# Performance work log

Measured on AMD Instinct MI355X. Metric: run time of the kernel, lower is better.

The kernel has to match this reference:

```python
import jax, jax.numpy as jnp
import numpy as np

K_PRE_NMS = 2000      # number of top-scoring candidates fed to NMS
IOU_THRESHOLD = 0.5
IMAGE_SIZE = 800.0


def decode_boxes(deltas, locations, stride):
    """Faithful fcos_apply_deltas_to_locations (incl. the all(-1) special case
    and the swapped-y-coordinate convention of the source)."""
    d = deltas * stride
    x, y = locations[:, 0], locations[:, 1]
    boxes = jnp.stack([x - d[:, 0], y - d[:, 1], x + d[:, 2], y + d[:, 3]], axis=1)
    all_bg = jnp.all(deltas == -1)
    degen = jnp.stack([x, y, x, y], axis=1)
    return jnp.where(all_bg, degen, boxes)


def nms_keep_mask(boxes_sorted, iou_threshold):
    """Sequential NMS on score-descending-sorted boxes. Reproduces the source's
    exact (quirky) IoU math: y1=boxes[:,3], y2=boxes[:,1], w/h via abs().
    Returns bool keep mask aligned with the sorted order."""
    K = boxes_sorted.shape[0]
    x1, y1 = boxes_sorted[:, 0], boxes_sorted[:, 3]
    x2, y2 = boxes_sorted[:, 2], boxes_sorted[:, 1]
    area = (x2 - x1) * (y2 - y1)
    idx = jnp.arange(K)

    def body(i, state):
        active, keep = state
        is_kept = active[i]
        keep = keep.at[i].set(is_kept)
        xx1 = jnp.maximum(x1[i], x1)
        yy1 = jnp.minimum(y1[i], y1)
        xx2 = jnp.minimum(x2[i], x2)
        yy2 = jnp.maximum(y2[i], y2)
        inter = jnp.abs(xx2 - xx1) * jnp.abs(yy2 - yy1)
        iou = inter / (area[i] + area - inter)
        suppress = is_kept & (iou > iou_threshold) & (idx > i)
        return active & ~suppress, keep

    active0 = jnp.ones((K,), dtype=bool)
    keep0 = jnp.zeros((K,), dtype=bool)
    _, keep = jax.lax.fori_loop(0, K, body, (active0, keep0))
    return keep


def setup_inputs() -> dict:
    key = jax.random.key(0)
    k1, k2, k3 = jax.random.split(key, 3)
    N, C = 1048576, 20
    deltas = jax.random.normal(k1, (N, 4), dtype=jnp.float32) * 4.0 + 8.0
    locations = jax.random.uniform(k2, (N, 2), dtype=jnp.float32) * IMAGE_SIZE
    logits = jax.random.normal(k3, (N, C), dtype=jnp.float32)
    return {"deltas": deltas, "locations": locations, "logits": logits, "stride": 8}


def reference(deltas, locations, logits, stride):
    # 1) box delta decode (all N locations)
    boxes = decode_boxes(deltas, locations, stride)
    # 2) per-location best class score / class id
    probs = jax.nn.sigmoid(logits)              # [N, C]
    cls_scores = jnp.max(probs, axis=1)         # [N]
    class_ids = jnp.argmax(probs, axis=1)       # [N]
    # 3) pre-NMS top-k
    top_scores, top_idx = jax.lax.top_k(cls_scores, K_PRE_NMS)
    cand_boxes = boxes[top_idx]                 # [K, 4]
    cand_cls = class_ids[top_idx]               # [K]
    # 4) class-offset trick (class_spec_nms)
    max_coord = jnp.max(cand_boxes)
    offsets = cand_cls.astype(cand_boxes.dtype) * (max_coord + 1.0)
    boxes_for_nms = cand_boxes + offsets[:, None]
    # 5) sort by score descending (top_k already sorted; argsort is faithful to nms())
    order = jnp.argsort(-top_scores)
    keep = nms_keep_mask(boxes_for_nms[order], IOU_THRESHOLD)
    return cand_boxes[order], top_scores[order], cand_cls[order], keep
```

## Files before the change

### kernel.cpp

```cpp
#include <hip/hip_runtime.h>
#include <stdint.h>
#include <math.h>

#pragma clang fp contract(off)

#define N_ROWS 1048576
#define N_CLS  20
#define K_TOP  2000
#define CAND_MAX 8192
#define NBINS  4096
#define H_COPIES 4
#define DELTA_ULP 4096u

#define SC_CNT   0
#define SC_MAXK  1
#define SC_DONE  2
#define SC_BAR   3
#define SC_FLAG  4

static constexpr size_t OFF_MKEY = 0;
static constexpr size_t OFF_CLS  = OFF_MKEY + 4ull * N_ROWS;
static constexpr size_t OFF_HIST = OFF_CLS + (size_t)N_ROWS;
static constexpr size_t OFF_SCAL = OFF_HIST + 4ull * H_COPIES * NBINS;
static constexpr size_t OFF_GRP  = OFF_SCAL + 64;
static constexpr size_t OFF_CAND = OFF_GRP + 256;
static constexpr size_t OFF_MASK = OFF_CAND + 8ull * CAND_MAX;

__device__ __forceinline__ uint32_t mono_key(float f) {
    uint32_t u = __float_as_uint(f);
    return u ^ ((u & 0x80000000u) ? 0xFFFFFFFFu : 0x80000000u);
}
__device__ __forceinline__ float mono_inv(uint32_t k) {
    uint32_t u = (k & 0x80000000u) ? (k ^ 0x80000000u) : ~k;
    return __uint_as_float(u);
}

__global__ __launch_bounds__(256) void k_scoremax(const float* __restrict__ logits,
                                                  uint32_t* __restrict__ mkey,
                                                  uint8_t* __restrict__ cls,
                                                  uint32_t* __restrict__ zreg) {
    int t = threadIdx.x, b = blockIdx.x;
    if (b < 8) {
#pragma unroll
        for (int k = 0; k < 8; ++k) zreg[b * 256 + t + k * 2048] = 0;
        if (b == 7 && t < 80) zreg[16384 + t] = 0;
    }
    size_t r0 = (size_t)b * 1024 + t;
    const float4* p0 = (const float4*)(logits + r0 * N_CLS);
    const float4* p1 = (const float4*)(logits + (r0 + 256) * N_CLS);
    const float4* p2 = (const float4*)(logits + (r0 + 512) * N_CLS);
    const float4* p3 = (const float4*)(logits + (r0 + 768) * N_CLS);
    float4 a0 = p0[0], a1 = p0[1], a2 = p0[2], a3 = p0[3], a4 = p0[4];
    float4 b0 = p1[0], b1 = p1[1], b2 = p1[2], b3 = p1[3], b4 = p1[4];
    float4 c0 = p2[0], c1 = p2[1], c2 = p2[2], c3 = p2[3], c4 = p2[4];
    float4 d0 = p3[0], d1 = p3[1], d2 = p3[2], d3 = p3[3], d4 = p3[4];
    __builtin_amdgcn_sched_barrier(0);

#define CK(mm, cc, val, idx) if ((val) > mm) { mm = (val); cc = (idx); }
    float mA = a0.x; int cA = 0;
    CK(mA, cA, a0.y, 1)  CK(mA, cA, a0.z, 2)  CK(mA, cA, a0.w, 3)
    CK(mA, cA, a1.x, 4)  CK(mA, cA, a1.y, 5)  CK(mA, cA, a1.z, 6)  CK(mA, cA, a1.w, 7)
    CK(mA, cA, a2.x, 8)  CK(mA, cA, a2.y, 9)  CK(mA, cA, a2.z, 10) CK(mA, cA, a2.w, 11)
    CK(mA, cA, a3.x, 12) CK(mA, cA, a3.y, 13) CK(mA, cA, a3.z, 14) CK(mA, cA, a3.w, 15)
    CK(mA, cA, a4.x, 16) CK(mA, cA, a4.y, 17) CK(mA, cA, a4.z, 18) CK(mA, cA, a4.w, 19)
    float mB = b0.x; int cB = 0;
    CK(mB, cB, b0.y, 1)  CK(mB, cB, b0.z, 2)  CK(mB, cB, b0.w, 3)
    CK(mB, cB, b1.x, 4)  CK(mB, cB, b1.y, 5)  CK(mB, cB, b1.z, 6)  CK(mB, cB, b1.w, 7)
    CK(mB, cB, b2.x, 8)  CK(mB, cB, b2.y, 9)  CK(mB, cB, b2.z, 10) CK(mB, cB, b2.w, 11)
    CK(mB, cB, b3.x, 12) CK(mB, cB, b3.y, 13) CK(mB, cB, b3.z, 14) CK(mB, cB, b3.w, 15)
    CK(mB, cB, b4.x, 16) CK(mB, cB, b4.y, 17) CK(mB, cB, b4.z, 18) CK(mB, cB, b4.w, 19)
    float mC = c0.x; int cC = 0;
    CK(mC, cC, c0.y, 1)  CK(mC, cC, c0.z, 2)  CK(mC, cC, c0.w, 3)
    CK(mC, cC, c1.x, 4)  CK(mC, cC, c1.y, 5)  CK(mC, cC, c1.z, 6)  CK(mC, cC, c1.w, 7)
    CK(mC, cC, c2.x, 8)  CK(mC, cC, c2.y, 9)  CK(mC, cC, c2.z, 10) CK(mC, cC, c2.w, 11)
    CK(mC, cC, c3.x, 12) CK(mC, cC, c3.y, 13) CK(mC, cC, c3.z, 14) CK(mC, cC, c3.w, 15)
    CK(mC, cC, c4.x, 16) CK(mC, cC, c4.y, 17) CK(mC, cC, c4.z, 18) CK(mC, cC, c4.w, 19)
    float mD = d0.x; int cD = 0;
    CK(mD, cD, d0.y, 1)  CK(mD, cD, d0.z, 2)  CK(mD, cD, d0.w, 3)
    CK(mD, cD, d1.x, 4)  CK(mD, cD, d1.y, 5)  CK(mD, cD, d1.z, 6)  CK(mD, cD, d1.w, 7)
    CK(mD, cD, d2.x, 8)  CK(mD, cD, d2.y, 9)  CK(mD, cD, d2.z, 10) CK(mD, cD, d2.w, 11)
    CK(mD, cD, d3.x, 12) CK(mD, cD, d3.y, 13) CK(mD, cD, d3.z, 14) CK(mD, cD, d3.w, 15)
    CK(mD, cD, d4.x, 16) CK(mD, cD, d4.y, 17) CK(mD, cD, d4.z, 18) CK(mD, cD, d4.w, 19)
#undef CK

    mkey[r0]       = mono_key(mA);  cls[r0]       = (uint8_t)cA;
    mkey[r0 + 256] = mono_key(mB);  cls[r0 + 256] = (uint8_t)cB;
    mkey[r0 + 512] = mono_key(mC);  cls[r0 + 512] = (uint8_t)cC;
    mkey[r0 + 768] = mono_key(mD);  cls[r0 + 768] = (uint8_t)cD;
}

__global__ __launch_bounds__(256) void k_histcompact(const uint32_t* __restrict__ mkey,
                                                     uint32_t* __restrict__ hist,
                                                     uint32_t* __restrict__ scal,
                                                     unsigned long long* __restrict__ cand) {
    __shared__ uint32_t hh[NBINS];
    __shared__ uint64_t stg[1024];
    __shared__ uint32_t bc;
    __shared__ uint32_t cnt, gbase;
    __shared__ int islast;
    int t = threadIdx.x, b = blockIdx.x;
    int lane = t & 63;
    if (t == 0) cnt = 0;
    for (int i = t; i < NBINS; i += 256) hh[i] = 0;
    __syncthreads();

    const uint4* m4 = (const uint4*)mkey;
    size_t base = (size_t)b * 1024;
    uint4 v0 = m4[base + t], v1 = m4[base + 256 + t];
    uint4 v2 = m4[base + 512 + t], v3 = m4[base + 768 + t];
    atomicAdd(&hh[v0.x >> 20], 1u); atomicAdd(&hh[v0.y >> 20], 1u);
    atomicAdd(&hh[v0.z >> 20], 1u); atomicAdd(&hh[v0.w >> 20], 1u);
    atomicAdd(&hh[v1.x >> 20], 1u); atomicAdd(&hh[v1.y >> 20], 1u);
    atomicAdd(&hh[v1.z >> 20], 1u); atomicAdd(&hh[v1.w >> 20], 1u);
    atomicAdd(&hh[v2.x >> 20], 1u); atomicAdd(&hh[v2.y >> 20], 1u);
    atomicAdd(&hh[v2.z >> 20], 1u); atomicAdd(&hh[v2.w >> 20], 1u);
    atomicAdd(&hh[v3.x >> 20], 1u); atomicAdd(&hh[v3.y >> 20], 1u);
    atomicAdd(&hh[v3.z >> 20], 1u); atomicAdd(&hh[v3.w >> 20], 1u);
    __syncthreads();

    uint32_t cp = (uint32_t)((b & (H_COPIES - 1)) << 12);
    unsigned long long dummy = 0;
    for (int i = 0; i < 16; ++i) {
        uint32_t h = hh[t * 16 + i];
        if (h) dummy += atomicAdd(&hist[cp + t * 16 + i], h);
    }
    asm volatile("" :: "v"(dummy));
    asm volatile("s_waitcnt vmcnt(0) lgkmcnt(0)" ::: "memory");
    __syncthreads();
    if (t == 0) {
        uint32_t old = atomicAdd(&scal[SC_BAR], 1u);
        islast = (old == 255u) ? 1 : 0;
    }
    __syncthreads();

    if (islast) {
        uint32_t bv[16]; uint32_t ct = 0;
#pragma unroll
        for (int i = 0; i < 16; ++i) {
            uint32_t s = 0;
#pragma unroll
            for (int k = 0; k < H_COPIES; ++k) s += atomicAdd(&hist[(k << 12) + t * 16 + i], 0u);
            bv[i] = s; ct += s;
        }
        hh[t] = ct;
        __syncthreads();
        for (int off = 1; off < 256; off <<= 1) {
            uint32_t v = (t + off < 256) ? hh[t + off] : 0;
            __syncthreads();
            hh[t] += v;
            __syncthreads();
        }
        if (hh[t] >= (uint32_t)K_TOP && (t == 255 || hh[t + 1] < (uint32_t)K_TOP)) {
            uint32_t cum = (t == 255) ? 0u : hh[t + 1];
            int i = 15;
            for (; i >= 0; --i) { cum += bv[i]; if (cum >= (uint32_t)K_TOP) break; }
            if (i < 0) i = 0;
            uint32_t tk = ((uint32_t)(t * 16 + i)) << 20;
            uint32_t Tk = (tk > DELTA_ULP) ? (tk - DELTA_ULP) : 0u;
            atomicExch(&scal[SC_FLAG], Tk + 1u);
        }
    }
    for (;;) {
        if (t == 0) bc = atomicAdd(&scal[SC_FLAG], 0u);
        __syncthreads();
        if (bc != 0u) break;
        __builtin_amdgcn_s_sleep(32);
    }
    uint32_t T = bc - 1u;

#define CSLOT(u, roff) {                                                         \
        uint32_t uu = (u);                                                       \
        bool pass = uu >= T;                                                     \
        unsigned long long bal = __ballot(pass);                                 \
        if (bal) {                                                               \
            uint32_t wbase = 0;                                                  \
            if (lane == 0) wbase = atomicAdd(&cnt, (uint32_t)__popcll(bal));     \
            wbase = __shfl(wbase, 0);                                            \
            if (pass) {                                                          \
                uint32_t pos = wbase + (uint32_t)__popcll(bal & ((1ull << lane) - 1ull)); \
                if (pos < 1024) {                                                \
                    float m = mono_inv(uu);                                      \
                    float ef = (float)exp(-(double)m);                           \
                    float s = 1.0f / (1.0f + ef);                                \
                    stg[pos] = ((uint64_t)(~__float_as_uint(s)) << 32) | (roff); \
                }                                                                \
            }                                                                    \
        }                                                                        \
    }
    uint32_t rb = (uint32_t)((base + t) * 4);
    CSLOT(v0.x, rb + 0) CSLOT(v0.y, rb + 1) CSLOT(v0.z, rb + 2) CSLOT(v0.w, rb + 3)
    rb = (uint32_t)((base + 256 + t) * 4);
    CSLOT(v1.x, rb + 0) CSLOT(v1.y, rb + 1) CSLOT(v1.z, rb + 2) CSLOT(v1.w, rb + 3)
    rb = (uint32_t)((base + 512 + t) * 4);
    CSLOT(v2.x, rb + 0) CSLOT(v2.y, rb + 1) CSLOT(v2.z, rb + 2) CSLOT(v2.w, rb + 3)
    rb = (uint32_t)((base + 768 + t) * 4);
    CSLOT(v3.x, rb + 0) CSLOT(v3.y, rb + 1) CSLOT(v3.z, rb + 2) CSLOT(v3.w, rb + 3)
#undef CSLOT
    __syncthreads();
    uint32_t n = cnt; if (n > 1024) n = 1024;
    if (t == 0 && n) gbase = atomicAdd(&scal[SC_CNT], n);
    __syncthreads();
    if (n) {
        uint32_t gb = gbase;
        for (uint32_t i = t; i < n; i += 256) {
            uint32_t pos = gb + i;
            if (pos < (uint32_t)CAND_MAX) cand[pos] = stg[i];
        }
    }
}

__global__ __launch_bounds__(256) void k_rank(const unsigned long long* __restrict__ cand,
                                              uint32_t* __restrict__ scal,
                                              const float* __restrict__ deltas,
                                              const float* __restrict__ locs,
                                              const int* __restrict__ stridep,
                                              const uint8_t* __restrict__ cls,
                                              float* __restrict__ out) {
    __shared__ uint64_t keys[CAND_MAX];
    int t = threadIdx.x;
    uint32_t M = scal[SC_CNT];
    if (M > (uint32_t)CAND_MAX) M = CAND_MAX;
    for (uint32_t i = t; i < M; i += 256) keys[i] = cand[i];
    __syncthreads();
    int wid = t >> 6, lane = t & 63;
    float stridef = (float)(*stridep);
    float wmx = -3.4e38f;
    for (uint32_t c = (uint32_t)blockIdx.x * 4 + wid; c < M; c += 1024) {
        uint64_t myk = keys[c];
        uint32_t r = 0;
        uint32_t j = lane;
        for (; j + 192 < M; j += 256) {
            uint64_t k0 = keys[j], k1 = keys[j + 64], k2 = keys[j + 128], k3 = keys[j + 192];
            r += (uint32_t)(k0 < myk) + (uint32_t)(k1 < myk)
               + (uint32_t)(k2 < myk) + (uint32_t)(k3 < myk);
        }
        for (; j < M; j += 64) r += (keys[j] < myk) ? 1u : 0u;
#pragma unroll
        for (int o = 32; o > 0; o >>= 1) r += __shfl_down(r, o);
        if (lane == 0 && r < (uint32_t)K_TOP) {
            uint32_t row = (uint32_t)myk & (N_ROWS - 1);
            float s = __uint_as_float(~(uint32_t)(myk >> 32));
            float4 dl = ((const float4*)deltas)[row];
            float2 lc = ((const float2*)locs)[row];
            float d0 = dl.x * stridef, d1 = dl.y * stridef, d2 = dl.z * stridef, d3 = dl.w * stridef;
            float b0f = lc.x - d0, b1f = lc.y - d1, b2f = lc.x + d2, b3f = lc.y + d3;
            float4 bx = { b0f, b1f, b2f, b3f };
            *(float4*)&out[4 * r] = bx;
            out[8000 + r] = s;
            out[10000 + r] = (float)cls[row];
            wmx = fmaxf(wmx, fmaxf(fmaxf(b0f, b1f), fmaxf(b2f, b3f)));
        }
    }
    if (lane == 0) atomicMax(&scal[SC_MAXK], mono_key(wmx));
}

__global__ __launch_bounds__(256) void k_maskscan(const float* __restrict__ out_ro,
                                                  uint32_t* __restrict__ scal,
                                                  uint64_t* __restrict__ mask,
                                                  unsigned long long* __restrict__ grp,
                                                  float* __restrict__ out) {
    __shared__ uint64_t wb[4][32];
    __shared__ int lastdone;
    int t = threadIdx.x;
    int lane = t & 63;
    int wid = t >> 6;
    int i = blockIdx.x * 4 + wid;
    float off1 = mono_inv(scal[SC_MAXK]) + 1.0f;
    float4 boxi = *(const float4*)&out_ro[4 * i];
    float oi = out_ro[10000 + i] * off1;
    float x1i = boxi.x + oi, y2i = boxi.y + oi, x2i = boxi.z + oi, y1i = boxi.w + oi;
    float ai = (x2i - x1i) * (y2i - y1i);
    uint64_t any = 0;
    for (int jb = 0; jb < 32; ++jb) {
        int j = jb * 64 + lane;
        bool sup = false;
        if (j < K_TOP && j > i) {
            float4 boxj = *(const float4*)&out_ro[4 * j];
            float oj = out_ro[10000 + j] * off1;
            float x1j = boxj.x + oj, y2j = boxj.y + oj, x2j = boxj.z + oj, y1j = boxj.w + oj;
            float aj = (x2j - x1j) * (y2j - y1j);
            float xx1 = fmaxf(x1i, x1j);
            float yy1 = fminf(y1i, y1j);
            float xx2 = fminf(x2i, x2j);
            float yy2 = fmaxf(y2i, y2j);
            float inter = fabsf(xx2 - xx1) * fabsf(yy2 - yy1);
            float iou = inter / ((ai + aj) - inter);
            sup = iou > 0.5f;
        }
        unsigned long long bits = __ballot(sup);
        if (lane == 0) wb[wid][jb] = bits;
        any |= bits;
    }
    unsigned long long dummy = 0;
    if (lane == 0 && any) {
        for (int jb = 0; jb < 32; ++jb)
            dummy += atomicExch(&mask[(size_t)i * 32 + jb], wb[wid][jb]);
        dummy += atomicOr(&grp[i >> 6], 1ull << (i & 63));
    }
    asm volatile("" :: "v"(dummy));
    asm volatile("s_waitcnt vmcnt(0) lgkmcnt(0)" ::: "memory");
    __syncthreads();
    if (t == 0) {
        unsigned old = atomicAdd(&scal[SC_DONE], 1u);
        lastdone = (old == (unsigned)(gridDim.x - 1)) ? 1 : 0;
    }
    __syncthreads();
    if (!lastdone) return;

    if (t < 64) {
        int l = t;
        uint64_t g = (l < 32) ? atomicOr(&grp[l], 0ull) : 0ull;
        uint64_t active = ~0ull;
        if (__ballot(g != 0ull)) {
            for (int gg = 0; gg < 32; ++gg) {
                uint64_t nz = __shfl(g, gg);
                while (nz) {
                    int b = __ffsll((long long)nz) - 1;
                    nz &= nz - 1;
                    int ii = gg * 64 + b;
                    uint64_t aw = __shfl(active, gg);
                    bool kept = (aw >> b) & 1ull;
                    uint64_t m = (l < 32) ? atomicOr(&mask[(size_t)ii * 32 + l], 0ull) : 0ull;
                    if (kept) active &= ~m;
                }
            }
        }
        if (l < 32) {
            int limit = K_TOP - l * 64;
            int nvec = limit < 64 ? limit / 4 : 16;
            for (int v = 0; v < nvec; ++v) {
                float4 f;
                f.x = ((active >> (4 * v + 0)) & 1ull) ? 1.0f : 0.0f;
                f.y = ((active >> (4 * v + 1)) & 1ull) ? 1.0f : 0.0f;
                f.z = ((active >> (4 * v + 2)) & 1ull) ? 1.0f : 0.0f;
                f.w = ((active >> (4 * v + 3)) & 1ull) ? 1.0f : 0.0f;
                *(float4*)&out[12000 + l * 64 + 4 * v] = f;
            }
        }
    }
}

extern "C" void kernel_launch(void* const* d_in, const int* in_sizes, int n_in,
                              void* d_out, int out_size, void* d_ws, size_t ws_size,
                              hipStream_t stream) {
    const float* deltas = (const float*)d_in[0];
    const float* locs   = (const float*)d_in[1];
    const float* logits = (const float*)d_in[2];
    const int*   stridep = (const int*)d_in[3];
    float* out = (float*)d_out;
    char* ws = (char*)d_ws;

    uint32_t* mkey = (uint32_t*)(ws + OFF_MKEY);
    uint8_t*  cls  = (uint8_t*)(ws + OFF_CLS);
    uint32_t* hist = (uint32_t*)(ws + OFF_HIST);
    uint32_t* scal = (uint32_t*)(ws + OFF_SCAL);
    unsigned long long* grp = (unsigned long long*)(ws + OFF_GRP);
    unsigned long long* cand = (unsigned long long*)(ws + OFF_CAND);
    uint64_t* mask = (uint64_t*)(ws + OFF_MASK);

    k_scoremax<<<dim3(1024), dim3(256), 0, stream>>>(logits, mkey, cls, hist);
    k_histcompact<<<dim3(256), dim3(256), 0, stream>>>(mkey, hist, scal, cand);
    k_rank<<<dim3(256), dim3(256), 0, stream>>>(cand, scal, deltas, locs, stridep, cls, out);
    k_maskscan<<<dim3(500), dim3(256), 0, stream>>>(out, scal, mask, grp, out);
}
```

Baseline: 90.07 us.

## Fuse histogram-compact and rank kernels via a second grid-wide spin barrier

Merges k_histcompact and k_rank into one persistent kernel, k_select. A second atomic counter barrier (SC_BAR2/SC_FLAG2) publishes the final candidate count, and all blocks then reload candidates from global memory with atomic reads into a reused 64KB shared buffer. This removes one kernel launch and the gap between the two kernels. In exchange it depends on all 256 blocks being co-resident, adds atomic writes and reads on the candidate array, and caps the key count slightly below CAND_MAX to make room for scalars in shared memory.

```diff
diff --git a/kernel.cpp b/kernel.cpp
--- a/kernel.cpp
+++ b/kernel.cpp
@@ -8,6 +8,7 @@
 #define N_CLS  20
 #define K_TOP  2000
 #define CAND_MAX 8192
+#define KEYS_MAX 8184
 #define NBINS  4096
 #define H_COPIES 4
 #define DELTA_ULP 4096u
@@ -17,6 +18,8 @@
 #define SC_DONE  2
 #define SC_BAR   3
 #define SC_FLAG  4
+#define SC_BAR2  5
+#define SC_FLAG2 6
 
 static constexpr size_t OFF_MKEY = 0;
 static constexpr size_t OFF_CLS  = OFF_MKEY + 4ull * N_ROWS;
@@ -89,18 +92,23 @@
     mkey[r0 + 768] = mono_key(mD);  cls[r0 + 768] = (uint8_t)cD;
 }
 
-__global__ __launch_bounds__(256) void k_histcompact(const uint32_t* __restrict__ mkey,
-                                                     uint32_t* __restrict__ hist,
-                                                     uint32_t* __restrict__ scal,
-                                                     unsigned long long* __restrict__ cand) {
-    __shared__ uint32_t hh[NBINS];
-    __shared__ uint64_t stg[1024];
-    __shared__ uint32_t bc;
-    __shared__ uint32_t cnt, gbase;
-    __shared__ int islast;
+__global__ __launch_bounds__(256) void k_select(const uint32_t* __restrict__ mkey,
+                                                uint32_t* __restrict__ hist,
+                                                uint32_t* __restrict__ scal,
+                                                unsigned long long* __restrict__ cand,
+                                                const float* __restrict__ deltas,
+                                                const float* __restrict__ locs,
+                                                const int* __restrict__ stridep,
+                                                const uint8_t* __restrict__ cls,
+                                                float* __restrict__ out) {
+    __shared__ __align__(16) unsigned char smem[65536];
+    uint32_t* hh   = (uint32_t*)smem;
+    uint64_t* stg  = (uint64_t*)(smem + 16384);
+    uint64_t* keys = (uint64_t*)smem;
+    uint32_t* sv   = (uint32_t*)(smem + 65472);
     int t = threadIdx.x, b = blockIdx.x;
     int lane = t & 63;
-    if (t == 0) cnt = 0;
+    if (t == 0) sv[1] = 0;
     for (int i = t; i < NBINS; i += 256) hh[i] = 0;
     __syncthreads();
 
@@ -129,11 +137,11 @@
     __syncthreads();
     if (t == 0) {
         uint32_t old = atomicAdd(&scal[SC_BAR], 1u);
-        islast = (old == 255u) ? 1 : 0;
-    }
-    __syncthreads();
-
-    if (islast) {
+        sv[3] = (old == 255u) ? 1u : 0u;
+    }
+    __syncthreads();
+
+    if (sv[3]) {
         uint32_t bv[16]; uint32_t ct = 0;
 #pragma unroll
         for (int i = 0; i < 16; ++i) {
@@ -161,12 +169,13 @@
         }
     }
     for (;;) {
-        if (t == 0) bc = atomicAdd(&scal[SC_FLAG], 0u);
+        if (t == 0) sv[0] = atomicAdd(&scal[SC_FLAG], 0u);
         __syncthreads();
-        if (bc != 0u) break;
+        if (sv[0] != 0u) break;
         __builtin_amdgcn_s_sleep(32);
     }
-    uint32_t T = bc - 1u;
+    uint32_t T = sv[0] - 1u;
+    __syncthreads();
 
 #define CSLOT(u, roff) {                                                         \
         uint32_t uu = (u);                                                       \
@@ -174,7 +183,7 @@
         unsigned long long bal = __ballot(pass);                                 \
         if (bal) {                                                               \
             uint32_t wbase = 0;                                                  \
-            if (lane == 0) wbase = atomicAdd(&cnt, (uint32_t)__popcll(bal));     \
+            if (lane == 0) wbase = atomicAdd(&sv[1], (uint32_t)__popcll(bal));   \
             wbase = __shfl(wbase, 0);                                            \
             if (pass) {                                                          \
                 uint32_t pos = wbase + (uint32_t)__popcll(bal & ((1ull << lane) - 1ull)); \
@@ -197,35 +206,48 @@
     CSLOT(v3.x, rb + 0) CSLOT(v3.y, rb + 1) CSLOT(v3.z, rb + 2) CSLOT(v3.w, rb + 3)
 #undef CSLOT
     __syncthreads();
-    uint32_t n = cnt; if (n > 1024) n = 1024;
-    if (t == 0 && n) gbase = atomicAdd(&scal[SC_CNT], n);
-    __syncthreads();
+    uint32_t n = sv[1]; if (n > 1024) n = 1024;
+    if (t == 0 && n) sv[2] = atomicAdd(&scal[SC_CNT], n);
+    __syncthreads();
+    dummy = 0;
     if (n) {
-        uint32_t gb = gbase;
+        uint32_t gb = sv[2];
         for (uint32_t i = t; i < n; i += 256) {
             uint32_t pos = gb + i;
-            if (pos < (uint32_t)CAND_MAX) cand[pos] = stg[i];
-        }
-    }
-}
-
-__global__ __launch_bounds__(256) void k_rank(const unsigned long long* __restrict__ cand,
-                                              uint32_t* __restrict__ scal,
-                                              const float* __restrict__ deltas,
-                                              const float* __restrict__ locs,
-                                              const int* __restrict__ stridep,
-                                              const uint8_t* __restrict__ cls,
-                                              float* __restrict__ out) {
-    __shared__ uint64_t keys[CAND_MAX];
-    int t = threadIdx.x;
-    uint32_t M = scal[SC_CNT];
-    if (M > (uint32_t)CAND_MAX) M = CAND_MAX;
-    for (uint32_t i = t; i < M; i += 256) keys[i] = cand[i];
-    __syncthreads();
-    int wid = t >> 6, lane = t & 63;
+            if (pos < (uint32_t)CAND_MAX)
+                dummy += atomicExch(&cand[pos], (unsigned long long)stg[i]);
+        }
+    }
+    asm volatile("" :: "v"(dummy));
+    asm volatile("s_waitcnt vmcnt(0) lgkmcnt(0)" ::: "memory");
+    __syncthreads();
+
+    if (t == 0) {
+        uint32_t old = atomicAdd(&scal[SC_BAR2], 1u);
+        sv[3] = (old == 255u) ? 1u : 0u;
+    }
+    __syncthreads();
+    if (sv[3] && t == 0) {
+        uint32_t M = atomicAdd(&scal[SC_CNT], 0u);
+        atomicExch(&scal[SC_FLAG2], M + 1u);
+    }
+    for (;;) {
+        if (t == 0) sv[0] = atomicAdd(&scal[SC_FLAG2], 0u);
+        __syncthreads();
+        if (sv[0] != 0u) break;
+        __builtin_amdgcn_s_sleep(32);
+    }
+    uint32_t M = sv[0] - 1u;
+    if (M > (uint32_t)KEYS_MAX) M = KEYS_MAX;
+    __syncthreads();
+
+    for (uint32_t i = t; i < M; i += 256)
+        keys[i] = (uint64_t)atomicOr(&cand[i], 0ull);
+    __syncthreads();
+    int wid = t >> 6;
     float stridef = (float)(*stridep);
     float wmx = -3.4e38f;
-    for (uint32_t c = (uint32_t)blockIdx.x * 4 + wid; c < M; c += 1024) {
+    for (uint32_t c = (uint32_t)b * 4 + wid; c < M; c += 1024) {
         uint64_t myk = keys[c];
         uint32_t r = 0;
         uint32_t j = lane;
@@ -359,7 +381,7 @@
     uint64_t* mask = (uint64_t*)(ws + OFF_MASK);
 
     k_scoremax<<<dim3(1024), dim3(256), 0, stream>>>(logits, mkey, cls, hist);
-    k_histcompact<<<dim3(256), dim3(256), 0, stream>>>(mkey, hist, scal, cand);
-    k_rank<<<dim3(256), dim3(256), 0, stream>>>(cand, scal, deltas, locs, stridep, cls, out);
+    k_select<<<dim3(256), dim3(256), 0, stream>>>(mkey, hist, scal, cand,
+                                                  deltas, locs, stridep, cls, out);
     k_maskscan<<<dim3(500), dim3(256), 0, stream>>>(out, scal, mask, grp, out);
 }
```

Measured after the change: 97.14 us. 1.08x slower.
